# Performance work log

Measured on AMD Instinct MI355X. Metric: run time of the kernel, lower is better.

Reference implementation:

```python
import jax, jax.numpy as jnp
import numpy as np

HIDDEN = 1024
HEADS = 16
HEAD_DIM = HIDDEN // HEADS


def setup_inputs() -> dict:
    key = jax.random.key(0)
    kx, kw = jax.random.split(key)
    x = jax.random.normal(kx, (1, 4096, HIDDEN), dtype=jnp.float32)
    # torch Linear weight is [out, in]; we store as [in, out] for x @ W
    W_qkv = jax.random.normal(kw, (HIDDEN, 3 * HIDDEN), dtype=jnp.float32) * (HIDDEN ** -0.5)
    return {"x": x, "W_qkv": W_qkv}


def reference(x, W_qkv):
    B, T, _ = x.shape
    qkv = x @ W_qkv                                    # [B, T, 3*HIDDEN]
    qkv = qkv.reshape(B, T, 3, HEADS, HEAD_DIM)
    qkv = jnp.transpose(qkv, (2, 0, 3, 1, 4))          # [3, B, H, T, Dh]
    q, k, v = qkv[0], qkv[1], qkv[2]
    scale = HEAD_DIM ** -0.5
    attn = jnp.einsum("bhqd,bhkd->bhqk", q, k) * scale  # [B, H, T, T] materialized (naive)
    attn = jax.nn.softmax(attn, axis=-1)
    out = jnp.einsum("bhqk,bhkd->bhqd", attn, v)        # [B, H, T, Dh]
    out = jnp.transpose(out, (0, 2, 1, 3)).reshape(B, T, HIDDEN)
    return out
```

## Files before the change

kernel.cpp:

```cpp
#include <hip/hip_runtime.h>

#define SEQ 4096
#define HID 1024
#define NH  16
#define DH  64
#define N3  3072

typedef __attribute__((ext_vector_type(4))) float floatx4;
typedef __attribute__((ext_vector_type(8))) short shortx8;
typedef __attribute__((ext_vector_type(4))) short shortx4;

__device__ __forceinline__ short f2bf(float f) {
    return (short)((__builtin_bit_cast(unsigned, f) + 0x8000u) >> 16);
}
__device__ __forceinline__ unsigned pk2bf(float a, float b) {
    unsigned ua = __builtin_bit_cast(unsigned, a) + 0x8000u;
    unsigned ub = __builtin_bit_cast(unsigned, b) + 0x8000u;
    return (ua >> 16) | (ub & 0xFFFF0000u);
}
__device__ __forceinline__ shortx4 pk4bf(float a, float b, float c, float d) {
    union { unsigned u[2]; shortx4 s; } x;
    x.u[0] = pk2bf(a, b);
    x.u[1] = pk2bf(c, d);
    return x.s;
}

__device__ __forceinline__ unsigned cvtpk(float lo, float hi) {
    unsigned r;
    asm("v_cvt_pk_bf16_f32 %0, %1, %2" : "=v"(r) : "v"(lo), "v"(hi));
    return r;
}

#if __has_builtin(__builtin_amdgcn_exp2f)
#define fexp2 __builtin_amdgcn_exp2f
#else
#define fexp2 exp2f
#endif

#define mfma32 __builtin_amdgcn_mfma_f32_16x16x32_bf16

__device__ __forceinline__ void gll16(const short* g, short* l) {
    __builtin_amdgcn_global_load_lds(
        (const __attribute__((address_space(1))) unsigned*)g,
        (__attribute__((address_space(3))) unsigned*)l, 16, 0, 0);
}

__global__ __launch_bounds__(256) void convert_x(
    const float* __restrict__ x, short* __restrict__ Xb)
{
    size_t i = (size_t)blockIdx.x * 256 + threadIdx.x;
    float4 v = *(const float4*)&x[i * 4];
    shortx4 b = pk4bf(v.x, v.y, v.z, v.w);
    *(shortx4*)&Xb[i * 4] = b;
}

__global__ __launch_bounds__(256) void transpose_W(
    const float* __restrict__ W, short* __restrict__ Wt)
{
    __shared__ short Ws[128 * 40];
    const int t  = threadIdx.x;
    const int n0 = blockIdx.x * 128;
    const int k0 = blockIdx.y * 32;
    #pragma unroll
    for (int i = 0; i < 4; i++) {
        int idx = t + i * 256;
        int k = idx >> 5, c4 = idx & 31;
        float4 v = *(const float4*)&W[(size_t)(k0 + k) * N3 + n0 + c4 * 4];
        Ws[(c4 * 4 + 0) * 40 + k] = f2bf(v.x);
        Ws[(c4 * 4 + 1) * 40 + k] = f2bf(v.y);
        Ws[(c4 * 4 + 2) * 40 + k] = f2bf(v.z);
        Ws[(c4 * 4 + 3) * 40 + k] = f2bf(v.w);
    }
    __syncthreads();
    #pragma unroll
    for (int i = 0; i < 2; i++) {
        int idx = t + i * 256;
        int n = idx >> 2, seg = idx & 3;
        shortx8 g = *(const shortx8*)&Ws[n * 40 + seg * 8];
        *(shortx8*)&Wt[(size_t)(n0 + n) * HID + k0 + seg * 8] = g;
    }
}

#define LDC 136
__global__ __launch_bounds__(256) void qkv_gemm(
    const short* __restrict__ Xb, const short* __restrict__ Wt,
    short* __restrict__ Qb, short* __restrict__ Kb, short* __restrict__ Vt)
{
    __shared__ short SM[18432];
    short* As = SM;
    short* Bs = SM + 128 * 64;
    const int tid  = threadIdx.x;
    const int m0   = blockIdx.x * 128;
    const int n0   = blockIdx.y * 128;
    const int lane = tid & 63;
    const int wid  = tid >> 6;
    const int wm   = (wid >> 1) * 64;
    const int wn   = (wid & 1) * 64;
    const int l15  = lane & 15;
    const int quad = lane >> 4;

    floatx4 acc[4][4];
    #pragma unroll
    for (int i = 0; i < 4; i++)
        #pragma unroll
        for (int j = 0; j < 4; j++)
            acc[i][j] = (floatx4){0.f, 0.f, 0.f, 0.f};

    const int arow = tid >> 3, ac = tid & 7;
    const int swk  = (ac ^ (arow & 7)) << 3;
    const short* ag = Xb + (size_t)(m0 + arow) * HID + swk;
    const short* bg = Wt + (size_t)(n0 + arow) * HID + swk;
    short* al = As + (size_t)(tid & 192) * 8;
    short* bl = Bs + (size_t)(tid & 192) * 8;
    const int r7 = l15 & 7;

    for (int k0 = 0; k0 < HID; k0 += 64) {
        #pragma unroll
        for (int i = 0; i < 4; i++)
            gll16(ag + (size_t)i * 32 * HID + k0, al + i * 2048);
        #pragma unroll
        for (int i = 0; i < 4; i++)
            gll16(bg + (size_t)i * 32 * HID + k0, bl + i * 2048);
        __syncthreads();
        #pragma unroll
        for (int kh = 0; kh < 2; kh++) {
            shortx8 af[4], bf[4];
            #pragma unroll
            for (int t = 0; t < 4; t++) {
                int R = wm + t * 16 + l15;
                af[t] = *(const shortx8*)&As[(R << 6) + ((((kh << 2) + quad) ^ r7) << 3)];
                int Rb = wn + t * 16 + l15;
                bf[t] = *(const shortx8*)&Bs[(Rb << 6) + ((((kh << 2) + quad) ^ r7) << 3)];
            }
            #pragma unroll
            for (int tm = 0; tm < 4; tm++)
                #pragma unroll
                for (int tn = 0; tn < 4; tn++)
                    acc[tm][tn] = mfma32(af[tm], bf[tn], acc[tm][tn], 0, 0, 0);
        }
        __syncthreads();
    }

    short* Cs = SM;
    const float sc = (n0 < 1024) ? 0.18033688011112042f : 1.0f;
    #pragma unroll
    for (int tm = 0; tm < 4; tm++)
        #pragma unroll
        for (int tn = 0; tn < 4; tn++)
            #pragma unroll
            for (int r = 0; r < 4; r++)
                Cs[(wm + tm * 16 + quad * 4 + r) * LDC + wn + tn * 16 + l15] =
                    f2bf(acc[tm][tn][r] * sc);
    __syncthreads();
    const int h0 = (n0 & 1023) >> 6;
    if (n0 < 2048) {
        short* base = (n0 < 1024) ? Qb : Kb;
        #pragma unroll
        for (int j = 0; j < 8; j++) {
            int idx = tid + j * 256;
            int row = idx >> 4, col = (idx & 15) * 8;
            shortx8 v = *(const shortx8*)&Cs[row * LDC + col];
            *(shortx8*)&base[((size_t)(h0 + (col >> 6)) * SEQ + m0 + row) * DH + (col & 63)] = v;
        }
    } else {
        #pragma unroll
        for (int j = 0; j < 8; j++) {
            int idx = tid + j * 256;
            int col = idx >> 4;
            int t8  = (idx & 15) * 8;
            shortx8 v;
            #pragma unroll
            for (int k = 0; k < 8; k++) v[k] = Cs[(t8 + k) * LDC + col];
            *(shortx8*)&Vt[((size_t)(h0 + (col >> 6)) * DH + (col & 63)) * SEQ + m0 + t8] = v;
        }
    }
}

__global__ __launch_bounds__(256, 3) void flash_attn(
    const short* __restrict__ Qb, const short* __restrict__ Kb,
    const short* __restrict__ Vt, float* __restrict__ out,
    float* __restrict__ Opart, float* __restrict__ Lpart,
    int kpc, int nit, int final)
{
    __shared__ short Ks[2][4096];
    __shared__ short Vs[2][4096];
    const int tid  = threadIdx.x;
    const int wid  = tid >> 6;
    const int lane = tid & 63;
    const int l15  = lane & 15;
    const int quad = lane >> 4;

    const int nblk = (int)(gridDim.x * gridDim.y * gridDim.z);
    const int lin  = (int)blockIdx.x + ((int)blockIdx.y << 4) + ((int)blockIdx.z << 8);
    const int work = (lin & 7) * (nblk >> 3) + (lin >> 3);
    const int h    = (work >> 4) & 15;
    const int ch   = work >> 8;
    const int q0   = (work & 15) * 256 + wid * 64;
    const int tstart = ch * kpc;
    const shortx8 ones8 = {(short)0x3F80, (short)0x3F80, (short)0x3F80, (short)0x3F80,
                           (short)0x3F80, (short)0x3F80, (short)0x3F80, (short)0x3F80};
    const floatx4 z4 = {0.f, 0.f, 0.f, 0.f};

    shortx8 qf[4][2];
    #pragma unroll
    for (int s = 0; s < 4; s++) {
        const short* qp = Qb + ((size_t)h * SEQ + q0 + s * 16 + l15) * DH;
        qf[s][0] = *(const shortx8*)(qp + quad * 8);
        qf[s][1] = *(const shortx8*)(qp + 32 + quad * 8);
    }

    floatx4 oacc[4][4];
    #pragma unroll
    for (int s = 0; s < 4; s++)
        #pragma unroll
        for (int dn = 0; dn < 4; dn++)
            oacc[s][dn] = z4;
    floatx4 lacc[4] = {z4, z4, z4, z4};

    const int rK   = tid >> 3, sK = tid & 7;
    const int key0 = 8 * ((rK >> 2) & 3) + 4 * ((rK >> 4) & 1) + (rK & 3);
    const int swo  = (sK ^ (rK & 7)) << 3;
    const short* kg = Kb + ((size_t)h * SEQ + tstart + key0) * DH + swo;
    const short* vg = Vt + ((size_t)h * DH + rK) * SEQ + tstart + swo;
    const int wslot = (tid & 192) * 8;

#define STAGE(b) do { \
        gll16(kg,            &Ks[b][wslot]); \
        gll16(kg + 32 * DH,  &Ks[b][wslot + 2048]); \
        gll16(vg,            &Vs[b][wslot]); \
        gll16(vg + 32 * SEQ, &Vs[b][wslot + 2048]); \
    } while (0)

    STAGE(0);
    kg += 64 * DH;  vg += 64;

    for (int it = 0; it < nit; it++) {
        __syncthreads();
        if (it + 1 < nit) {
            int b = (it + 1) & 1;
            STAGE(b);
            kg += 64 * DH;  vg += 64;
        }
        const short* ks = Ks[it & 1];
        const short* vs = Vs[it & 1];

        #pragma unroll
        for (int pair = 0; pair < 2; pair++) {
            int Ra = (pair * 2) * 16 + l15;
            int Rb = Ra + 16;
            int offa = (Ra << 6) + ((quad ^ (Ra & 7)) << 3);
            int offb = (Rb << 6) + ((quad ^ (Rb & 7)) << 3);
            shortx8 kf0a = *(const shortx8*)&ks[offa];
            shortx8 kf1a = *(const shortx8*)&ks[offa ^ 32];
            shortx8 kf0b = *(const shortx8*)&ks[offb];
            shortx8 kf1b = *(const shortx8*)&ks[offb ^ 32];
            floatx4 sta[4], stb[4];
            __builtin_amdgcn_s_setprio(1);
            #pragma unroll
            for (int s = 0; s < 4; s++) {
                floatx4 a = mfma32(kf0a, qf[s][0], z4, 0, 0, 0);
                a = mfma32(kf1a, qf[s][1], a, 0, 0, 0);
                sta[s] = a;
                floatx4 b = mfma32(kf0b, qf[s][0], z4, 0, 0, 0);
                b = mfma32(kf1b, qf[s][1], b, 0, 0, 0);
                stb[s] = b;
            }
            __builtin_amdgcn_s_setprio(0);
            union { unsigned u[4]; shortx8 s8; } pa[4];
            #pragma unroll
            for (int s = 0; s < 4; s++) {
                pa[s].u[0] = cvtpk(fexp2(sta[s][0]), fexp2(sta[s][1]));
                pa[s].u[1] = cvtpk(fexp2(sta[s][2]), fexp2(sta[s][3]));
                pa[s].u[2] = cvtpk(fexp2(stb[s][0]), fexp2(stb[s][1]));
                pa[s].u[3] = cvtpk(fexp2(stb[s][2]), fexp2(stb[s][3]));
            }
            __builtin_amdgcn_s_setprio(1);
            #pragma unroll
            for (int s = 0; s < 4; s++)
                lacc[s] = mfma32(pa[s].s8, ones8, lacc[s], 0, 0, 0);
            #pragma unroll
            for (int dn = 0; dn < 4; dn++) {
                int row = dn * 16 + l15;
                int off = ((row << 6) + ((quad ^ (row & 7)) << 3)) ^ (pair << 5);
                shortx8 vv = *(const shortx8*)&vs[off];
                #pragma unroll
                for (int s = 0; s < 4; s++)
                    oacc[s][dn] = mfma32(pa[s].s8, vv, oacc[s][dn], 0, 0, 0);
            }
            __builtin_amdgcn_s_setprio(0);
        }
    }
#undef STAGE

    if (final) {
        #pragma unroll
        for (int s = 0; s < 4; s++)
            #pragma unroll
            for (int r = 0; r < 4; r++) {
                float rl = 1.0f / lacc[s][r];
                int query = q0 + s * 16 + quad * 4 + r;
                float* d = out + (size_t)query * HID + h * DH + l15;
                #pragma unroll
                for (int dn = 0; dn < 4; dn++)
                    d[dn * 16] = oacc[s][dn][r] * rl;
            }
    } else {
        #pragma unroll
        for (int s = 0; s < 4; s++)
            #pragma unroll
            for (int r = 0; r < 4; r++) {
                int query = q0 + s * 16 + quad * 4 + r;
                float* d = Opart + ((size_t)ch * SEQ + query) * HID + h * DH + l15;
                #pragma unroll
                for (int dn = 0; dn < 4; dn++)
                    d[dn * 16] = oacc[s][dn][r];
            }
        if (l15 == 0) {
            float* lp = Lpart + ((size_t)ch * NH + h) * SEQ + q0;
            #pragma unroll
            for (int s = 0; s < 4; s++)
                #pragma unroll
                for (int r = 0; r < 4; r++)
                    lp[s * 16 + quad * 4 + r] = lacc[s][r];
        }
    }
}

__global__ __launch_bounds__(256) void combine(
    const float* __restrict__ Opart, const float* __restrict__ Lpart,
    float* __restrict__ out, int chn)
{
    size_t i = ((size_t)blockIdx.x * 256 + threadIdx.x) * 4;
    int q = (int)(i >> 10);
    int h = ((int)i & 1023) >> 6;
    float4 o = {0.f, 0.f, 0.f, 0.f};
    float l = 0.f;
    for (int c = 0; c < chn; c++) {
        float4 p = *(const float4*)&Opart[(size_t)c * SEQ * HID + i];
        o.x += p.x; o.y += p.y; o.z += p.z; o.w += p.w;
        l += Lpart[((size_t)c * NH + h) * SEQ + q];
    }
    float rl = 1.0f / l;
    float4 r = {o.x * rl, o.y * rl, o.z * rl, o.w * rl};
    *(float4*)&out[i] = r;
}

extern "C" void kernel_launch(void* const* d_in, const int* in_sizes, int n_in,
                              void* d_out, int out_size, void* d_ws, size_t ws_size,
                              hipStream_t stream) {
    const float* x = (const float*)d_in[0];
    const float* W = (const float*)d_in[1];
    float* out = (float*)d_out;

    short* Xb = (short*)d_ws;
    short* Wt = Xb + (size_t)SEQ * HID;
    short* Qb = Wt + (size_t)N3 * HID;
    short* Kb = Qb + (size_t)NH * SEQ * DH;
    short* Vt = Kb + (size_t)NH * SEQ * DH;
    float* Opart = (float*)(Vt + (size_t)NH * SEQ * DH);

    const size_t need4 = 39845888ull
                       + 4ull * SEQ * HID * 4
                       + 4ull * NH * SEQ * 4;
    const size_t need2 = 39845888ull + 2ull * SEQ * HID * 4 + 2ull * NH * SEQ * 4;
    const int chn = (ws_size >= need4) ? 4 : ((ws_size >= need2) ? 2 : 1);
    float* Lpart = Opart + (size_t)chn * SEQ * HID;
    const int kpc = SEQ / chn, nit = kpc / 64;

    convert_x  <<<dim3(SEQ * HID / 1024), 256, 0, stream>>>(x, Xb);
    transpose_W<<<dim3(N3 / 128, HID / 32), 256, 0, stream>>>(W, Wt);
    qkv_gemm   <<<dim3(SEQ / 128, N3 / 128), 256, 0, stream>>>(Xb, Wt, Qb, Kb, Vt);
    flash_attn <<<dim3(SEQ / 256, NH, chn), 256, 0, stream>>>(
        Qb, Kb, Vt, out, Opart, Lpart, kpc, nit, chn == 1);
    if (chn > 1)
        combine<<<dim3(SEQ * HID / 1024), 256, 0, stream>>>(Opart, Lpart, out, chn);
}
```

Baseline: 201.5 us.

## Merge prep kernels and split attention keys into three uneven chunks

The x conversion and W transpose are merged into one launch, which saves a kernel launch and lets both run at once. The flash attention key-split goes from 4 (or 2) chunks to 3 uneven chunks of 22/21/21 64-key tiles. The grid becomes 768 blocks, which may suit the CU count better, and the combine pass and partial buffers shrink. The chunk boundaries are now hardcoded for SEQ=4096.

```diff
diff --git a/kernel.cpp b/kernel.cpp
--- a/kernel.cpp
+++ b/kernel.cpp
@@ -45,22 +45,21 @@
         (__attribute__((address_space(3))) unsigned*)l, 16, 0, 0);
 }
 
-__global__ __launch_bounds__(256) void convert_x(
-    const float* __restrict__ x, short* __restrict__ Xb)
-{
-    size_t i = (size_t)blockIdx.x * 256 + threadIdx.x;
-    float4 v = *(const float4*)&x[i * 4];
-    shortx4 b = pk4bf(v.x, v.y, v.z, v.w);
-    *(shortx4*)&Xb[i * 4] = b;
-}
-
-__global__ __launch_bounds__(256) void transpose_W(
-    const float* __restrict__ W, short* __restrict__ Wt)
+__global__ __launch_bounds__(256) void prep(
+    const float* __restrict__ x, const float* __restrict__ W,
+    short* __restrict__ Xb, short* __restrict__ Wt)
 {
     __shared__ short Ws[128 * 40];
-    const int t  = threadIdx.x;
-    const int n0 = blockIdx.x * 128;
-    const int k0 = blockIdx.y * 32;
+    const int t = threadIdx.x;
+    if (blockIdx.x < 4096) {
+        size_t i = (size_t)blockIdx.x * 256 + t;
+        float4 v = *(const float4*)&x[i * 4];
+        *(shortx4*)&Xb[i * 4] = pk4bf(v.x, v.y, v.z, v.w);
+        return;
+    }
+    const int bx = (int)blockIdx.x - 4096;
+    const int n0 = (bx % 24) * 128;
+    const int k0 = (bx / 24) * 32;
     #pragma unroll
     for (int i = 0; i < 4; i++) {
         int idx = t + i * 256;
@@ -180,7 +179,7 @@
     const short* __restrict__ Qb, const short* __restrict__ Kb,
     const short* __restrict__ Vt, float* __restrict__ out,
     float* __restrict__ Opart, float* __restrict__ Lpart,
-    int kpc, int nit, int final)
+    int chn, int final)
 {
     __shared__ short Ks[2][4096];
     __shared__ short Vs[2][4096];
@@ -196,7 +195,8 @@
     const int h    = (work >> 4) & 15;
     const int ch   = work >> 8;
     const int q0   = (work & 15) * 256 + wid * 64;
-    const int tstart = ch * kpc;
+    const int nit    = (chn == 1) ? 64 : (ch == 0 ? 22 : 21);
+    const int tstart = (chn == 1) ? 0  : (ch == 0 ? 0 : 1408 + (ch - 1) * 1344);
     const shortx8 ones8 = {(short)0x3F80, (short)0x3F80, (short)0x3F80, (short)0x3F80,
                            (short)0x3F80, (short)0x3F80, (short)0x3F80, (short)0x3F80};
     const floatx4 z4 = {0.f, 0.f, 0.f, 0.f};
@@ -359,19 +359,16 @@
     short* Vt = Kb + (size_t)NH * SEQ * DH;
     float* Opart = (float*)(Vt + (size_t)NH * SEQ * DH);
 
-    const size_t need4 = 39845888ull
-                       + 4ull * SEQ * HID * 4
-                       + 4ull * NH * SEQ * 4;
-    const size_t need2 = 39845888ull + 2ull * SEQ * HID * 4 + 2ull * NH * SEQ * 4;
-    const int chn = (ws_size >= need4) ? 4 : ((ws_size >= need2) ? 2 : 1);
+    const size_t need3 = 39845888ull
+                       + 3ull * SEQ * HID * 4
+                       + 3ull * NH * SEQ * 4;
+    const int chn = (ws_size >= need3) ? 3 : 1;
     float* Lpart = Opart + (size_t)chn * SEQ * HID;
-    const int kpc = SEQ / chn, nit = kpc / 64;
-
-    convert_x  <<<dim3(SEQ * HID / 1024), 256, 0, stream>>>(x, Xb);
-    transpose_W<<<dim3(N3 / 128, HID / 32), 256, 0, stream>>>(W, Wt);
-    qkv_gemm   <<<dim3(SEQ / 128, N3 / 128), 256, 0, stream>>>(Xb, Wt, Qb, Kb, Vt);
-    flash_attn <<<dim3(SEQ / 256, NH, chn), 256, 0, stream>>>(
-        Qb, Kb, Vt, out, Opart, Lpart, kpc, nit, chn == 1);
+
+    prep      <<<dim3(4096 + 768), 256, 0, stream>>>(x, W, Xb, Wt);
+    qkv_gemm  <<<dim3(SEQ / 128, N3 / 128), 256, 0, stream>>>(Xb, Wt, Qb, Kb, Vt);
+    flash_attn<<<dim3(SEQ / 256, NH, chn), 256, 0, stream>>>(
+        Qb, Kb, Vt, out, Opart, Lpart, chn, chn == 1);
     if (chn > 1)
         combine<<<dim3(SEQ * HID / 1024), 256, 0, stream>>>(Opart, Lpart, out, chn);
 }
```

Measured after the change: 195.7 us. 1.03x faster.
